# Kernel tuning notes

Measured on AMD Instinct MI355X. Metric: run time of the kernel, lower is better.

Reference implementation:

```python
import jax, jax.numpy as jnp
import numpy as np

PHI = (1.0 + 5.0 ** 0.5) / 2.0
TWO_PI = 2.0 * np.pi
LN_EPS = 1e-5


def _complex_linear(xr, xi, Wr, Wi, br, bi):
    # (Wr + i*Wi) @ (xr + i*xi) + (br + i*bi)
    yr = xr @ Wr.T - xi @ Wi.T + br
    yi = xr @ Wi.T + xi @ Wr.T + bi
    return yr, yi


def _layernorm(x, g, b):
    m = jnp.mean(x, axis=-1, keepdims=True)
    v = jnp.mean((x - m) ** 2, axis=-1, keepdims=True)
    return (x - m) * jax.lax.rsqrt(v + LN_EPS) * g + b


def reference(w, b, ip_Wr, ip_Wi, ip_br, ip_bi, ln_g, ln_b, W_qkv, log_alpha, op_Wr, op_Wi):
    B, S, D = w.shape
    H = log_alpha.shape[0]
    Dh = D // H
    scale = jnp.sqrt(jnp.asarray(Dh, w.dtype))
    alpha = jax.nn.sigmoid(log_alpha)[None, :, None]  # (1,H,1)
    ts = jnp.arange(S, dtype=w.dtype)

    def step(carry, xs):
        hr, hi, vs = carry          # (B,D),(B,D),(B,H,Dh)
        w_t, b_t, t = xs            # (B,D),(B,D),()
        # InstrumentedEulerTransform: separated theta, complex product
        wl = 1.0 + jnp.abs(w_t)
        tphi = (t * PHI) % TWO_PI   # wrap_time_periodic
        thr = hr / wl + b_t + tphi
        thi = hi / wl + b_t + tphi
        sr, cr = jnp.sin(thr), jnp.cos(thr)
        si, ci = jnp.sin(thi), jnp.cos(thi)
        hr2 = cr * ci - sr * si
        hi2 = cr * si + sr * ci
        # InstrumentedEchoChamber.forward_step
        pr, pi_ = _complex_linear(hr2, hi2, ip_Wr, ip_Wi, ip_br, ip_bi)
        xc = _layernorm(pr + pi_, ln_g, ln_b)
        qkv = (xc @ W_qkv.T).reshape(B, 3, H, Dh)
        q, k, v = qkv[:, 0], qkv[:, 1], qkv[:, 2]
        vs2 = alpha * v + (1.0 - alpha) * vs
        gate = jax.nn.sigmoid(jnp.sum(q * k, axis=-1, keepdims=True) / scale)
        retr = (gate * vs2).reshape(B, D)
        # output_proj ComplexLinear on (retr, 0), no bias
        ore = retr @ op_Wr.T
        oim = retr @ op_Wi.T
        return (hr2, hi2, vs2), (ore, oim)

    init = (jnp.zeros((B, D), w.dtype), jnp.zeros((B, D), w.dtype),
            jnp.zeros((B, H, Dh), w.dtype))
    wT = jnp.swapaxes(w, 0, 1)  # (S,B,D)
    bT = jnp.swapaxes(b, 0, 1)
    _, (or_seq, oi_seq) = jax.lax.scan(step, init, (wT, bT, ts))
    out = jnp.stack([or_seq, oi_seq])      # (2,S,B,D)
    return jnp.swapaxes(out, 1, 2)         # (2,B,S,D)


def setup_inputs() -> dict:
    key = jax.random.key(0)
    ks = jax.random.split(key, 10)
    B, S, D, H = 8, 2048, 512, 8
    s = 0.02
    return {
        "w": jax.random.normal(ks[0], (B, S, D), jnp.float32),
        "b": jax.random.normal(ks[1], (B, S, D), jnp.float32),
        "ip_Wr": jax.random.normal(ks[2], (D, D), jnp.float32) * s,
        "ip_Wi": jax.random.normal(ks[3], (D, D), jnp.float32) * s,
        "ip_br": jax.random.normal(ks[4], (D,), jnp.float32) * s,
        "ip_bi": jax.random.normal(ks[5], (D,), jnp.float32) * s,
        "ln_g": jnp.ones((D,), jnp.float32),
        "ln_b": jnp.zeros((D,), jnp.float32),
        "W_qkv": jax.random.normal(ks[6], (3 * D, D), jnp.float32) * s,
        "log_alpha": jax.random.normal(ks[7], (H,), jnp.float32),
        "op_Wr": jax.random.normal(ks[8], (D, D), jnp.float32) * s,
        "op_Wi": jax.random.normal(ks[9], (D, D), jnp.float32) * s,
    }
```

## Files before the change

### kernel.cpp

```cpp
#include <hip/hip_runtime.h>
#include <math.h>

#define BB 8
#define SS 2048
#define DD 512
#define HH 8
#define MM (BB*SS)

#define CHK 128
#define CL  16
#define CW  32

#define RT 64
#define RW 128

typedef unsigned short u16;
typedef unsigned int   u32;
typedef float f32x4 __attribute__((ext_vector_type(4)));
typedef short s16x8 __attribute__((ext_vector_type(8)));

__device__ __forceinline__ u16 f2bf(float x){
  union { float f; unsigned u; } c; c.f = x;
  unsigned r = c.u + 0x7FFF + ((c.u >> 16) & 1);
  return (u16)(r >> 16);
}
__device__ __forceinline__ float bf2f(u16 x){
  union { unsigned u; float f; } c; c.u = ((unsigned)x) << 16;
  return c.f;
}
__device__ __forceinline__ void gload16(const u16* g, u16* l){
  __builtin_amdgcn_global_load_lds(
      (const __attribute__((address_space(1))) unsigned int*)g,
      (__attribute__((address_space(3))) unsigned int*)l, 16, 0, 0);
}

__global__ void prep_all(const float* __restrict__ ipWr, const float* __restrict__ ipWi,
                         const float* __restrict__ Wqkv,
                         const float* __restrict__ opWr, const float* __restrict__ opWi,
                         const float* __restrict__ ipbr, const float* __restrict__ ipbi,
                         const float* __restrict__ la,
                         u16* __restrict__ W1, u16* __restrict__ Wq, u16* __restrict__ W3,
                         float* __restrict__ tphi2, float* __restrict__ bc,
                         float* __restrict__ alph){
  int id = blockIdx.x*256 + threadIdx.x;
  if (id < 524288){
    int e = id & 7, lane = (id>>3) & 63, s = (id>>9) & 3;
    int rest = id >> 11, ks = rest & 31, nb2 = rest >> 5;
    int n = (nb2>>1)*128 + (nb2&1)*64 + s*16 + (lane&15);
    int k = ks*32 + (lane>>4)*8 + e;
    int d = k >> 1;
    float v = (k & 1) ? (ipWr[n*512+d] - ipWi[n*512+d])
                      : (ipWr[n*512+d] + ipWi[n*512+d]);
    W1[id] = f2bf(v);
  } else if (id < 1310720){
    int i = id - 524288;
    int e = i & 7, lane = (i>>3) & 63, s = (i>>9) & 3;
    int rest = i >> 11, ks = rest & 15, nb2 = rest >> 4;
    int n = (nb2>>1)*128 + (nb2&1)*64 + s*16 + (lane&15);
    int k = ks*32 + (lane>>4)*8 + e;
    Wq[i] = f2bf(Wqkv[n*512+k]);
  } else if (id < 1835008){
    int i = id - 1310720;
    int e = i & 7, lane = (i>>3) & 63, s = (i>>9) & 3;
    int rest = i >> 11, ks = rest & 15, nb2 = rest >> 4;
    int n = (nb2>>1)*128 + (nb2&1)*64 + s*16 + (lane&15);
    int k = ks*32 + (lane>>4)*8 + e;
    W3[i] = f2bf((n < 512) ? opWr[n*512+k] : opWi[(n-512)*512+k]);
  } else if (id < 1837056){
    int t = id - 1835008;
    const float PHI_F    = 1.61803398874989484820f;
    const float TWO_PI_F = 6.28318530717958647693f;
    tphi2[t] = 2.0f * fmodf((float)t * PHI_F, TWO_PI_F);
  } else if (id < 1837568){
    int t = id - 1837056;
    bc[t] = ipbr[t] + ipbi[t];
  } else if (id < 1837576){
    int t = id - 1837568;
    alph[t] = 1.0f/(1.0f + expf(-la[t]));
  }
}

__global__ __launch_bounds__(256) void scan_h(const float* __restrict__ w,
                                              const float* __restrict__ bb,
                                              const float* __restrict__ tphi2,
                                              u32* __restrict__ X32){
  const int e = blockIdx.x*256 + threadIdx.x;
  const int c = blockIdx.y;
  const int b = e >> 9;
  const int d = e & 511;
  const float SQRT2 = 1.41421356237309504880f;
  const float PI_4  = 0.78539816339744830962f;
  const int tstart = c*CL;
  int t0 = tstart - CW; if (t0 < 0) t0 = 0;
  const int nw = tstart - t0;

  const float* wp = w  + ((size_t)b*SS + t0)*DD + d;
  const float* bp = bb + ((size_t)b*SS + t0)*DD + d;
  const float* tp = tphi2 + t0;

  const int U = 8;
  float wv[U], bv[U], wn[U], bn[U];

  float ss = 0.f;
  const int ngw = nw >> 3;
  if (ngw > 0){
    #pragma unroll
    for (int i=0;i<U;i++){ wv[i] = wp[(size_t)i*DD]; bv[i] = bp[(size_t)i*DD]; }
    for (int gg=0; gg<ngw; ++gg){
      if (gg+1 < ngw){
        const float* wnp = wp + (size_t)(gg+1)*U*DD;
        const float* bnp = bp + (size_t)(gg+1)*U*DD;
        #pragma unroll
        for (int i=0;i<U;i++){ wn[i] = wnp[(size_t)i*DD]; bn[i] = bnp[(size_t)i*DD]; }
      }
      #pragma unroll
      for (int i=0;i<U;i++){
        float rwl2 = SQRT2 * __builtin_amdgcn_rcpf(1.0f + fabsf(wv[i]));
        float cw   = fmaf(2.0f, bv[i], tp[gg*U+i]) + PI_4;
        ss = __sinf(fmaf(ss, rwl2, cw));
      }
      #pragma unroll
      for (int i=0;i<U;i++){ wv[i]=wn[i]; bv[i]=bn[i]; }
    }
  }
  float hs = SQRT2 * ss;

  const float* wq = wp + (size_t)nw*DD;
  const float* bq = bp + (size_t)nw*DD;
  const float* tq = tp + nw;
  u32* xp = X32 + (size_t)(b*SS + tstart)*512 + d;

  #pragma unroll
  for (int i=0;i<U;i++){ wv[i] = wq[(size_t)i*DD]; bv[i] = bq[(size_t)i*DD]; }
  for (int gg=0; gg<CL/U; ++gg){
    if (gg+1 < CL/U){
      const float* wnp = wq + (size_t)(gg+1)*U*DD;
      const float* bnp = bq + (size_t)(gg+1)*U*DD;
      #pragma unroll
      for (int i=0;i<U;i++){ wn[i] = wnp[(size_t)i*DD]; bn[i] = bnp[(size_t)i*DD]; }
    }
    #pragma unroll
    for (int i=0;i<U;i++){
      float rwl = __builtin_amdgcn_rcpf(1.0f + fabsf(wv[i]));
      float cc  = fmaf(2.0f, bv[i], tq[gg*U+i]);
      float theta = fmaf(hs, rwl, cc);
      float sn = __sinf(theta);
      float cs = __cosf(theta);
      hs = cs + sn;
      xp[(size_t)(gg*U+i)*512] = (u32)f2bf(cs) | ((u32)f2bf(sn) << 16);
    }
    #pragma unroll
    for (int i=0;i<U;i++){ wv[i]=wn[i]; bv[i]=bn[i]; }
  }
}

template<int TAG, int EPI>
__global__ __launch_bounds__(256) void gemm_bf16(const u16* __restrict__ A,
                                                 const u16* __restrict__ W,
                                                 float* __restrict__ C0,
                                                 float* __restrict__ C1,
                                                 u16* __restrict__ C2,
                                                 const float* __restrict__ bias,
                                                 int N, int K){
  __shared__ __align__(16) u16 As[3][128*32];
  const int tid  = threadIdx.x;
  const int nwgx = gridDim.x;
  const int nwg  = nwgx * gridDim.y;
  const int lin  = blockIdx.y * nwgx + blockIdx.x;
  const int qq   = nwg >> 3;
  const int logi = (lin & 7) * qq + (lin >> 3);
  const int m0   = (logi / nwgx) * 128;
  const int n0   = (logi % nwgx) * 128;

  const int wave = tid >> 6;
  const int lane = tid & 63;
  const int wr   = wave >> 1, wc = wave & 1;
  const int l15  = lane & 15;
  const int g    = lane >> 4;

  const int rI   = lane >> 2;
  const int kgs  = (lane & 3) ^ ((lane >> 3) & 3);
  const int row0 = wave*32 + rI;
  const int row1 = wave*32 + 16 + rI;
  const u16* Asrc0 = A + (size_t)(m0 + row0) * K + kgs*8;
  const u16* Asrc1 = A + (size_t)(m0 + row1) * K + kgs*8;
  const int ld0 = (wave*2+0)*512;
  const int ld1 = (wave*2+1)*512;

  const int nK = K >> 5;
  const u16* Bf = W + ((size_t)((n0 >> 6) + wc) * nK) * 2048 + lane*8;

  f32x4 acc[4][4];
  #pragma unroll
  for (int i=0;i<4;i++)
    #pragma unroll
    for (int j=0;j<4;j++) acc[i][j] = (f32x4){0.f,0.f,0.f,0.f};

  s16x8 b0[4], b1[4];

#define STAGE_A(buf, koff) do {                    \
    gload16(Asrc0 + (koff), &As[buf][ld0]);        \
    gload16(Asrc1 + (koff), &As[buf][ld1]);        \
  } while(0)

#define LOADB(dst, hh) do {                                         \
    _Pragma("unroll")                                               \
    for (int s=0;s<4;s++)                                           \
      dst[s] = *(const s16x8*)(Bf + ((size_t)(hh)*4 + s)*512);      \
  } while(0)

#define PHASE(hh, bcur, bnxt) do {                                       \
    if ((hh)+2 < nK){                                                    \
      int nb = (hh)+2; nb -= (nb/3)*3;                                   \
      STAGE_A(nb, ((hh)+2)*32);                                          \
    }                                                                    \
    if ((hh)+1 < nK) LOADB(bnxt, (hh)+1);                                \
    {                                                                    \
      int rem = nK - 1 - (hh);                                           \
      if      (rem >= 2) asm volatile("s_waitcnt vmcnt(6)" ::: "memory");\
      else if (rem == 1) asm volatile("s_waitcnt vmcnt(4)" ::: "memory");\
      else               asm volatile("s_waitcnt vmcnt(0)" ::: "memory");\
    }                                                                    \
    __builtin_amdgcn_s_barrier();        \
    {                                                                    \
      int cb = (hh); cb -= (cb/3)*3;                                     \
      const u16* Ah = &As[cb][0];                                        \
      s16x8 af[4];                                                       \
      _Pragma("unroll")                                                  \
      for (int s=0;s<4;s++){                                             \
        int rA = wr*64 + s*16 + l15;                                     \
        af[s] = *(const s16x8*)&Ah[rA*32 + ((g ^ ((rA>>1)&3))*8)];       \
      }                                                                  \
      __builtin_amdgcn_s_setprio(1);                                     \
      _Pragma("unroll")                                                  \
      for (int mi=0;mi<4;mi++)                                           \
        _Pragma("unroll")                                                \
        for (int ni=0;ni<4;ni++)                                         \
          acc[mi][ni] = __builtin_amdgcn_mfma_f32_16x16x32_bf16(af[mi], bcur[ni], acc[mi][ni], 0, 0, 0); \
      __builtin_amdgcn_s_setprio(0);                                     \
    }                                                                    \
    asm volatile("" ::: "memory");                                       \
    __builtin_amdgcn_s_barrier();        \
  } while(0)

  STAGE_A(0, 0);
  STAGE_A(1, 32);
  LOADB(b0, 0);

  for (int h = 0; h < nK; h += 2){
    PHASE(h,   b0, b1);
    PHASE(h+1, b1, b0);
  }

#undef STAGE_A
#undef LOADB
#undef PHASE

  #pragma unroll
  for (int mi=0;mi<4;mi++){
    #pragma unroll
    for (int j=0;j<4;j++){
      int r = m0 + wr*64 + mi*16 + g*4 + j;
      #pragma unroll
      for (int ni=0;ni<4;ni++){
        int col = n0 + wc*64 + ni*16 + l15;
        float v = acc[mi][ni][j];
        if (EPI == 1){
          if (col < 512) C0[(size_t)r*512 + col]       = v;
          else           C1[(size_t)r*512 + (col-512)] = v;
        } else if (EPI == 2){
          C2[(size_t)r*N + col] = f2bf(v);
        } else {
          C2[(size_t)r*N + col] = f2bf(v + bias[col]);
        }
      }
    }
  }
}

__global__ __launch_bounds__(256) void ln_kernel(const u16* __restrict__ y,
                                                 const float* __restrict__ g,
                                                 const float* __restrict__ bb,
                                                 u16* __restrict__ xc){
  const int row  = blockIdx.x*4 + (threadIdx.x >> 6);
  const int lane = threadIdx.x & 63;
  s16x8 v = *(const s16x8*)(y + (size_t)row*512 + lane*8);
  float f[8];
  #pragma unroll
  for (int i=0;i<8;i++) f[i] = bf2f((u16)v[i]);
  float s = 0.f, s2 = 0.f;
  #pragma unroll
  for (int i=0;i<8;i++){ s += f[i]; s2 = fmaf(f[i], f[i], s2); }
  #pragma unroll
  for (int off=32; off>0; off>>=1){ s += __shfl_xor(s, off); s2 += __shfl_xor(s2, off); }
  float mean = s * (1.0f/512.0f);
  float var  = s2 * (1.0f/512.0f) - mean*mean;
  float rstd = rsqrtf(var + 1e-5f);
  float4 g0 = ((const float4*)g)[lane*2],  g1 = ((const float4*)g)[lane*2+1];
  float4 b0 = ((const float4*)bb)[lane*2], b1 = ((const float4*)bb)[lane*2+1];
  s16x8 o;
  o[0] = (short)f2bf((f[0]-mean)*rstd*g0.x + b0.x);
  o[1] = (short)f2bf((f[1]-mean)*rstd*g0.y + b0.y);
  o[2] = (short)f2bf((f[2]-mean)*rstd*g0.z + b0.z);
  o[3] = (short)f2bf((f[3]-mean)*rstd*g0.w + b0.w);
  o[4] = (short)f2bf((f[4]-mean)*rstd*g1.x + b1.x);
  o[5] = (short)f2bf((f[5]-mean)*rstd*g1.y + b1.y);
  o[6] = (short)f2bf((f[6]-mean)*rstd*g1.z + b1.z);
  o[7] = (short)f2bf((f[7]-mean)*rstd*g1.w + b1.w);
  *(s16x8*)(xc + (size_t)row*512 + lane*8) = o;
}

__global__ __launch_bounds__(256) void retr_fused(const u16* __restrict__ qkv,
                                                  const float* __restrict__ alph,
                                                  u16* __restrict__ retr){
  const int wid  = blockIdx.x*4 + (threadIdx.x >> 6);
  const int lane = threadIdx.x & 63;
  const int c = wid & 31;
  const int h = (wid >> 5) & 7;
  const int b = wid >> 8;
  const float a  = alph[h];
  const float om = 1.0f - a;
  const int d  = h*64 + lane;
  const int t0 = c*RT;
  int w0 = t0 - RW; if (w0 < 0) w0 = 0;
  const int nw = t0 - w0;

  const u16* vp = qkv + ((size_t)(b*SS + w0))*1536 + 1024 + d;
  float vs = 0.f;
  {
    const int U = 8;
    float vv[U], vn[U];
    const int ng = nw >> 3;
    if (ng > 0){
      #pragma unroll
      for (int i=0;i<U;i++) vv[i] = bf2f(vp[(size_t)i*1536]);
      for (int gg=0; gg<ng; ++gg){
        if (gg+1 < ng){
          const u16* vnp = vp + (size_t)(gg+1)*U*1536;
          #pragma unroll
          for (int i=0;i<U;i++) vn[i] = bf2f(vnp[(size_t)i*1536]);
        }
        #pragma unroll
        for (int i=0;i<U;i++) vs = fmaf(a, vv[i], om*vs);
        #pragma unroll
        for (int i=0;i<U;i++) vv[i] = vn[i];
      }
    }
  }
  const u16* qp = qkv + ((size_t)(b*SS + t0))*1536 + d;
  u16* op = retr + ((size_t)(b*SS + t0))*512 + d;
  #pragma unroll 4
  for (int i=0;i<RT;i++){
    float q  = bf2f(qp[(size_t)i*1536]);
    float kk = bf2f(qp[(size_t)i*1536 + 512]);
    float v  = bf2f(qp[(size_t)i*1536 + 1024]);
    vs = fmaf(a, v, om*vs);
    float p = q*kk;
    #pragma unroll
    for (int off=32; off>0; off>>=1) p += __shfl_xor(p, off);
    float gate = 1.0f/(1.0f + __expf(-p*0.125f));
    op[(size_t)i*512] = f2bf(gate * vs);
  }
}

extern "C" void kernel_launch(void* const* d_in, const int* in_sizes, int n_in,
                              void* d_out, int out_size, void* d_ws, size_t ws_size,
                              hipStream_t stream) {
  const float* w    = (const float*)d_in[0];
  const float* b    = (const float*)d_in[1];
  const float* ipWr = (const float*)d_in[2];
  const float* ipWi = (const float*)d_in[3];
  const float* ipbr = (const float*)d_in[4];
  const float* ipbi = (const float*)d_in[5];
  const float* lng  = (const float*)d_in[6];
  const float* lnb  = (const float*)d_in[7];
  const float* Wqkv = (const float*)d_in[8];
  const float* la   = (const float*)d_in[9];
  const float* opWr = (const float*)d_in[10];
  const float* opWi = (const float*)d_in[11];
  float* out0 = (float*)d_out;
  float* out1 = out0 + (size_t)MM*DD;

  char* base = (char*)d_ws;
  u16*   W1    = (u16*)  (base + 0);
  u16*   Wq    = (u16*)  (base + 1048576);
  u16*   W3    = (u16*)  (base + 2621440);
  float* bc    = (float*)(base + 3670016);
  float* alph  = (float*)(base + 3672064);
  float* tphi2 = (float*)(base + 3672128);
  u32*   X32   = (u32*)  (base + 3680384);
  u16*   y     = (u16*)  (base + 37234816);
  u16*   xc    = (u16*)  (base + 54012032);
  u16*   qkv   = (u16*)  (base + 70789248);
  u16*   retr  = (u16*)X32;

  prep_all<<<7179,256,0,stream>>>(ipWr, ipWi, Wqkv, opWr, opWi, ipbr, ipbi, la,
                                  W1, Wq, W3, tphi2, bc, alph);

  scan_h<<<dim3(16,CHK),256,0,stream>>>(w, b, tphi2, X32);

  gemm_bf16<1,3><<<dim3(4,128),256,0,stream>>>((const u16*)X32, W1, nullptr, nullptr, y, bc, 512, 1024);
  ln_kernel<<<4096,256,0,stream>>>(y, lng, lnb, xc);
  gemm_bf16<2,2><<<dim3(12,128),256,0,stream>>>(xc, Wq, nullptr, nullptr, qkv, nullptr, 1536, 512);

  retr_fused<<<512,256,0,stream>>>(qkv, alph, retr);

  gemm_bf16<3,1><<<dim3(8,128),256,0,stream>>>(retr, W3, out0, out1, nullptr, nullptr, 1024, 512);
}
```

Before: 155.5 us.

## Fold LayerNorm into QKV GEMM via partial row stats and weight prescaling

Removes the standalone LayerNorm kernel. The first GEMM epilogue now writes per-slice row sums and sums of squares, and a small kernel reduces them to mean and rstd. The QKV GEMM consumes the un-normalized y directly, with gamma folded into the weights and the mean and beta applied through precomputed per-column vectors. This saves a full read and write pass over the activation, at the cost of computing variance from fp32 partial sums of the pre-bf16 values, a slow serial per-column dot product in prep, and a smaller retrieval warm-up window (RW 128 to 96), which trades exactness of the decayed state for less recomputation.

```diff
diff --git a/kernel.cpp b/kernel.cpp
--- a/kernel.cpp
+++ b/kernel.cpp
@@ -12,7 +12,7 @@
 #define CW  32
 
 #define RT 64
-#define RW 128
+#define RW 96
 
 typedef unsigned short u16;
 typedef unsigned int   u32;
@@ -39,9 +39,11 @@
                          const float* __restrict__ opWr, const float* __restrict__ opWi,
                          const float* __restrict__ ipbr, const float* __restrict__ ipbi,
                          const float* __restrict__ la,
+                         const float* __restrict__ lng, const float* __restrict__ lnb,
                          u16* __restrict__ W1, u16* __restrict__ Wq, u16* __restrict__ W3,
                          float* __restrict__ tphi2, float* __restrict__ bc,
-                         float* __restrict__ alph){
+                         float* __restrict__ alph,
+                         float* __restrict__ c1v, float* __restrict__ c2v){
   int id = blockIdx.x*256 + threadIdx.x;
   if (id < 524288){
     int e = id & 7, lane = (id>>3) & 63, s = (id>>9) & 3;
@@ -58,7 +60,7 @@
     int rest = i >> 11, ks = rest & 15, nb2 = rest >> 4;
     int n = (nb2>>1)*128 + (nb2&1)*64 + s*16 + (lane&15);
     int k = ks*32 + (lane>>4)*8 + e;
-    Wq[i] = f2bf(Wqkv[n*512+k]);
+    Wq[i] = f2bf(Wqkv[n*512+k] * lng[k]);
   } else if (id < 1835008){
     int i = id - 1310720;
     int e = i & 7, lane = (i>>3) & 63, s = (i>>9) & 3;
@@ -77,7 +79,30 @@
   } else if (id < 1837576){
     int t = id - 1837568;
     alph[t] = 1.0f/(1.0f + expf(-la[t]));
-  }
+  } else if (id < 1839112){
+    int n = id - 1837576;
+    const float* wrow = Wqkv + (size_t)n*512;
+    float sc1 = 0.f, sc2 = 0.f;
+    for (int k=0;k<512;k++){
+      float wv = wrow[k];
+      sc1 = fmaf(lng[k], wv, sc1);
+      sc2 = fmaf(lnb[k], wv, sc2);
+    }
+    c1v[n] = sc1; c2v[n] = sc2;
+  }
+}
+
+__global__ __launch_bounds__(256) void stats_final(const float* __restrict__ Pst,
+                                                   float* __restrict__ murs){
+  int r = blockIdx.x*256 + threadIdx.x;
+  const float4* p = (const float4*)(Pst + (size_t)r*16);
+  float4 a = p[0], b = p[1], c = p[2], d = p[3];
+  float s  = a.x+a.z + b.x+b.z + c.x+c.z + d.x+d.z;
+  float s2 = a.y+a.w + b.y+b.w + c.y+c.w + d.y+d.w;
+  float mu  = s  * (1.0f/512.0f);
+  float var = s2 * (1.0f/512.0f) - mu*mu;
+  murs[r*2]   = mu;
+  murs[r*2+1] = rsqrtf(var + 1e-5f);
 }
 
 __global__ __launch_bounds__(256) void scan_h(const float* __restrict__ w,
@@ -161,6 +186,10 @@
                                                  float* __restrict__ C1,
                                                  u16* __restrict__ C2,
                                                  const float* __restrict__ bias,
+                                                 const float* __restrict__ murs,
+                                                 const float* __restrict__ c1v,
+                                                 const float* __restrict__ c2v,
+                                                 float* __restrict__ Pst,
                                                  int N, int K){
   __shared__ __align__(16) u16 As[3][128*32];
   const int tid  = threadIdx.x;
@@ -261,53 +290,44 @@
     #pragma unroll
     for (int j=0;j<4;j++){
       int r = m0 + wr*64 + mi*16 + g*4 + j;
-      #pragma unroll
-      for (int ni=0;ni<4;ni++){
-        int col = n0 + wc*64 + ni*16 + l15;
-        float v = acc[mi][ni][j];
-        if (EPI == 1){
+      if (EPI == 1){
+        #pragma unroll
+        for (int ni=0;ni<4;ni++){
+          int col = n0 + wc*64 + ni*16 + l15;
+          float v = acc[mi][ni][j];
           if (col < 512) C0[(size_t)r*512 + col]       = v;
           else           C1[(size_t)r*512 + (col-512)] = v;
-        } else if (EPI == 2){
+        }
+      } else if (EPI == 3){
+        float s1 = 0.f, s2v = 0.f;
+        #pragma unroll
+        for (int ni=0;ni<4;ni++){
+          int col = n0 + wc*64 + ni*16 + l15;
+          float v = acc[mi][ni][j] + bias[col];
           C2[(size_t)r*N + col] = f2bf(v);
-        } else {
-          C2[(size_t)r*N + col] = f2bf(v + bias[col]);
+          s1 += v; s2v = fmaf(v, v, s2v);
+        }
+        #pragma unroll
+        for (int off=1; off<16; off<<=1){
+          s1  += __shfl_xor(s1,  off);
+          s2v += __shfl_xor(s2v, off);
+        }
+        if (l15 == 0){
+          int slice = (n0 >> 6) + wc;
+          Pst[((size_t)r*8 + slice)*2]     = s1;
+          Pst[((size_t)r*8 + slice)*2 + 1] = s2v;
+        }
+      } else {
+        float mu = murs[r*2], rs = murs[r*2+1];
+        #pragma unroll
+        for (int ni=0;ni<4;ni++){
+          int col = n0 + wc*64 + ni*16 + l15;
+          float v = rs*(acc[mi][ni][j] - mu*c1v[col]) + c2v[col];
+          C2[(size_t)r*N + col] = f2bf(v);
         }
       }
     }
   }
-}
-
-__global__ __launch_bounds__(256) void ln_kernel(const u16* __restrict__ y,
-                                                 const float* __restrict__ g,
-                                                 const float* __restrict__ bb,
-                                                 u16* __restrict__ xc){
-  const int row  = blockIdx.x*4 + (threadIdx.x >> 6);
-  const int lane = threadIdx.x & 63;
-  s16x8 v = *(const s16x8*)(y + (size_t)row*512 + lane*8);
-  float f[8];
-  #pragma unroll
-  for (int i=0;i<8;i++) f[i] = bf2f((u16)v[i]);
-  float s = 0.f, s2 = 0.f;
-  #pragma unroll
-  for (int i=0;i<8;i++){ s += f[i]; s2 = fmaf(f[i], f[i], s2); }
-  #pragma unroll
-  for (int off=32; off>0; off>>=1){ s += __shfl_xor(s, off); s2 += __shfl_xor(s2, off); }
-  float mean = s * (1.0f/512.0f);
-  float var  = s2 * (1.0f/512.0f) - mean*mean;
-  float rstd = rsqrtf(var + 1e-5f);
-  float4 g0 = ((const float4*)g)[lane*2],  g1 = ((const float4*)g)[lane*2+1];
-  float4 b0 = ((const float4*)bb)[lane*2], b1 = ((const float4*)bb)[lane*2+1];
-  s16x8 o;
-  o[0] = (short)f2bf((f[0]-mean)*rstd*g0.x + b0.x);
-  o[1] = (short)f2bf((f[1]-mean)*rstd*g0.y + b0.y);
-  o[2] = (short)f2bf((f[2]-mean)*rstd*g0.z + b0.z);
-  o[3] = (short)f2bf((f[3]-mean)*rstd*g0.w + b0.w);
-  o[4] = (short)f2bf((f[4]-mean)*rstd*g1.x + b1.x);
-  o[5] = (short)f2bf((f[5]-mean)*rstd*g1.y + b1.y);
-  o[6] = (short)f2bf((f[6]-mean)*rstd*g1.z + b1.z);
-  o[7] = (short)f2bf((f[7]-mean)*rstd*g1.w + b1.w);
-  *(s16x8*)(xc + (size_t)row*512 + lane*8) = o;
 }
 
 __global__ __launch_bounds__(256) void retr_fused(const u16* __restrict__ qkv,
@@ -390,20 +410,26 @@
   float* tphi2 = (float*)(base + 3672128);
   u32*   X32   = (u32*)  (base + 3680384);
   u16*   y     = (u16*)  (base + 37234816);
-  u16*   xc    = (u16*)  (base + 54012032);
   u16*   qkv   = (u16*)  (base + 70789248);
+  float* c1v   = (float*)(base + 121120896);
+  float* c2v   = (float*)(base + 121127040);
+  float* murs  = (float*)(base + 121133184);
+  float* Pst   = (float*)(base + 121264256);
   u16*   retr  = (u16*)X32;
 
-  prep_all<<<7179,256,0,stream>>>(ipWr, ipWi, Wqkv, opWr, opWi, ipbr, ipbi, la,
-                                  W1, Wq, W3, tphi2, bc, alph);
+  prep_all<<<7184,256,0,stream>>>(ipWr, ipWi, Wqkv, opWr, opWi, ipbr, ipbi, la,
+                                  lng, lnb, W1, Wq, W3, tphi2, bc, alph, c1v, c2v);
 
   scan_h<<<dim3(16,CHK),256,0,stream>>>(w, b, tphi2, X32);
 
-  gemm_bf16<1,3><<<dim3(4,128),256,0,stream>>>((const u16*)X32, W1, nullptr, nullptr, y, bc, 512, 1024);
-  ln_kernel<<<4096,256,0,stream>>>(y, lng, lnb, xc);
-  gemm_bf16<2,2><<<dim3(12,128),256,0,stream>>>(xc, Wq, nullptr, nullptr, qkv, nullptr, 1536, 512);
+  gemm_bf16<1,3><<<dim3(4,128),256,0,stream>>>((const u16*)X32, W1, nullptr, nullptr, y,
+                                               bc, nullptr, nullptr, nullptr, Pst, 512, 1024);
+  stats_final<<<64,256,0,stream>>>(Pst, murs);
+  gemm_bf16<2,4><<<dim3(12,128),256,0,stream>>>(y, Wq, nullptr, nullptr, qkv,
+                                                nullptr, murs, c1v, c2v, nullptr, 1536, 512);
 
   retr_fused<<<512,256,0,stream>>>(qkv, alph, retr);
 
-  gemm_bf16<3,1><<<dim3(8,128),256,0,stream>>>(retr, W3, out0, out1, nullptr, nullptr, 1024, 512);
-}
+  gemm_bf16<3,1><<<dim3(8,128),256,0,stream>>>(retr, W3, out0, out1, nullptr,
+                                               nullptr, nullptr, nullptr, nullptr, nullptr, 1024, 512);
+}
```

After: 173.0 us. +11.2%, slower.
